# Optimization experiments

Measured on AMD Instinct MI355X. Metric: run time of the kernel, lower is better.

The kernel has to match this reference:

```python
import jax, jax.numpy as jnp
import numpy as np

ALPHA = 0.2   # LeakyReLU negative slope
OF = 64       # out_features


def setup_inputs() -> dict:
    key = jax.random.key(0)
    k1, k2, k3, k4 = jax.random.split(key, 4)
    h = jax.random.normal(k1, (16, 2048, 12, 128), dtype=jnp.float32)
    adj = jax.random.randint(k2, (2, 6, 6), 0, 2, dtype=jnp.int32)
    # learned params (xavier-like scale)
    W = jax.random.normal(k3, (128, 64), dtype=jnp.float32) * 0.1
    a = jax.random.normal(k4, (2, 2 * OF, 1), dtype=jnp.float32) * 0.1
    return {"h": h, "adj": adj, "W": W, "a": a}


def reference(h, adj, W, a):
    # h: [B, N, 12, Fin], adj: [2, 6, 6], W: [Fin, OF], a: [2, 2*OF, 1]
    Wh = jnp.einsum('bnkf,fo->bnko', h, W)  # [B, N, 12, OF]
    outs = []
    for i in range(2):  # fixed 2 chunks of 6 nodes (h.shape[2] // 6)
        chunk = Wh[:, :, i * 6:(i + 1) * 6, :]       # [B, N, 6, OF]
        # matmul(a_input, a[i]) decomposes: e_pq = a1.Wh_p + a2.Wh_q
        a1 = a[i, :OF, 0]
        a2 = a[i, OF:, 0]
        s1 = chunk @ a1                               # [B, N, 6]
        s2 = chunk @ a2                               # [B, N, 6]
        e = jax.nn.leaky_relu(s1[..., :, None] + s2[..., None, :], ALPHA)  # [B,N,6,6]
        ei = e[i]                                     # NOTE: batch index i, as in source
        att = jnp.where(adj[i] > 0, ei, jnp.float32(-9e15))  # [N, 6, 6]
        att = jax.nn.softmax(att, axis=-1)
        # dropout omitted (eval mode)
        outs.append(jnp.einsum('npq,bnqf->bnpf', att, chunk))  # [B, N, 6, OF]
    h_prime = jnp.concatenate(outs, axis=2)           # [B, N, 12, OF]
    return jax.nn.elu(h_prime)                        # concat=True -> ELU
```

## Files before the change

kernel.cpp:

```cpp
#include <hip/hip_runtime.h>
#include <math.h>

#define LRELU_ALPHA 0.2f
#define NEG_BIG -9000000000000000.0f

#define WA_OFF 147456
#define WF_OFF 147968

typedef __attribute__((ext_vector_type(8))) short bf16x8;
typedef __attribute__((ext_vector_type(4))) float f32x4;

static __device__ inline unsigned short f2bf(float x) {
    unsigned int u = __float_as_uint(x);
    unsigned int r = (u + 0x7FFFu + ((u >> 16) & 1u)) >> 16;
    return (unsigned short)r;
}

__global__ __launch_bounds__(256) void gat_prep_kernel(
    const float* __restrict__ W, const float* __restrict__ a,
    float* __restrict__ ws)
{
    const int tid = threadIdx.x;
    if (blockIdx.x < 32) {
        short* wf = (short*)(ws + WF_OFF);
        const int o = blockIdx.x * 256 + tid;
        const int n = o >> 7, k = o & 127;
        wf[o] = (short)f2bf(W[k * 64 + n]);
    } else {
        float* wa = ws + WA_OFF;
        for (int idx = tid; idx < 512; idx += 256) {
            const int gi = idx >> 8, j = (idx >> 7) & 1, c = idx & 127;
            const float* Wr = W + c * 64;
            const float* ar = a + gi * 128 + j * 64;
            float s = 0.f;
#pragma unroll
            for (int f = 0; f < 64; ++f) s = fmaf(Wr[f], ar[f], s);
            wa[idx] = s;
        }
    }
}

__global__ __launch_bounds__(256) void gat_att_kernel(
    const float* __restrict__ h, const int* __restrict__ adj,
    float* __restrict__ ws)
{
    const int warp = threadIdx.x >> 6;
    const int lane = threadIdx.x & 63;
    const int iw = blockIdx.x * 4 + warp;
    const int gi = iw >> 11;
    const int n  = iw & 2047;

    const float* wa = ws + WA_OFF;
    const float2 w1 = *(const float2*)(wa + gi * 256 + 2 * lane);
    const float2 w2 = *(const float2*)(wa + gi * 256 + 128 + 2 * lane);
    const float* hp = h + ((size_t)(gi * 2048 + n) * 12 + (size_t)gi * 6) * 128 + 2 * lane;

    float t1[6], t2[6];
#pragma unroll
    for (int q = 0; q < 6; ++q) {
        const float2 hq = *(const float2*)(hp + q * 128);
        t1[q] = hq.x * w1.x + hq.y * w1.y;
        t2[q] = hq.x * w2.x + hq.y * w2.y;
    }
#pragma unroll
    for (int off = 32; off > 0; off >>= 1) {
#pragma unroll
        for (int q = 0; q < 6; ++q) {
            t1[q] += __shfl_xor(t1[q], off, 64);
            t2[q] += __shfl_xor(t2[q], off, 64);
        }
    }

    if (lane < 6) {
        const int p = lane;
        float s1p = t1[0];
#pragma unroll
        for (int q = 1; q < 6; ++q) { if (p == q) s1p = t1[q]; }

        float row[6];
        float mx = -3.0e38f;
#pragma unroll
        for (int q = 0; q < 6; ++q) {
            float e = s1p + t2[q];
            e = (e > 0.f) ? e : (LRELU_ALPHA * e);
            const int ad = adj[gi * 36 + p * 6 + q];
            const float m = (ad > 0) ? e : NEG_BIG;
            row[q] = m;
            mx = fmaxf(mx, m);
        }
        float sum = 0.f;
#pragma unroll
        for (int q = 0; q < 6; ++q) {
            row[q] = expf(row[q] - mx);
            sum += row[q];
        }
        const float inv = 1.f / sum;
        float* op = ws + (size_t)iw * 36 + p * 6;
#pragma unroll
        for (int q = 0; q < 6; ++q) op[q] = row[q] * inv;
    }
}

#define PSTR 136
__global__ __launch_bounds__(256, 8) void gat_main_mfma(
    const float* __restrict__ h, const float* __restrict__ ws,
    float* __restrict__ out)
{
    __shared__ __align__(16) short Pl[48 * PSTR];
    __shared__ __align__(16) float attl[288];

    const int tid  = threadIdx.x;
    const int warp = tid >> 6;
    const int lane = tid & 63;
    const int half = lane >> 5;
    const int li   = lane & 31;
    const int bn0  = blockIdx.x * 4;
    const int n0   = bn0 & 2047;

    for (int i = tid; i < 288; i += 256) {
        const int gi = i / 144;
        const int rem = i - gi * 144;
        const int nn = rem / 36;
        const int e  = rem - nn * 36;
        attl[i] = ws[(size_t)(gi * 2048 + n0 + nn) * 36 + e];
    }

    const int bn = bn0 + warp;
    const int gi = half;
    const float* hb = h + (size_t)bn * 1536 + gi * 6 * 128 + li * 4;
    f32x4 hv[6];
#pragma unroll
    for (int r = 0; r < 6; ++r)
        hv[r] = __builtin_nontemporal_load((const f32x4*)(hb + r * 128));

    __syncthreads();

    const float* av = attl + gi * 144 + warp * 36;
#pragma unroll
    for (int p = 0; p < 6; ++p) {
        float ax = 0.f, ay = 0.f, az = 0.f, aw = 0.f;
#pragma unroll
        for (int q = 0; q < 6; ++q) {
            const float apq = av[p * 6 + q];
            const f32x4 hq = hv[q];
            ax = fmaf(apq, hq[0], ax);
            ay = fmaf(apq, hq[1], ay);
            az = fmaf(apq, hq[2], az);
            aw = fmaf(apq, hq[3], aw);
        }
        const int row = warp * 12 + gi * 6 + p;
        ushort4 pk;
        pk.x = f2bf(ax); pk.y = f2bf(ay);
        pk.z = f2bf(az); pk.w = f2bf(aw);
        *(ushort4*)(Pl + row * PSTR + li * 4) = pk;
    }

    __syncthreads();

    const short* wf = (const short*)(ws + WF_OFF);
    const int col  = lane & 15;
    const int quad = lane >> 4;
    f32x4 acc[3];
#pragma unroll
    for (int mt = 0; mt < 3; ++mt) acc[mt] = (f32x4){0.f, 0.f, 0.f, 0.f};

#pragma unroll
    for (int ks = 0; ks < 4; ++ks) {
        const bf16x8 bfr = *(const bf16x8*)(wf + (warp * 16 + col) * 128 + ks * 32 + quad * 8);
#pragma unroll
        for (int mt = 0; mt < 3; ++mt) {
            const bf16x8 afr = *(const bf16x8*)(Pl + (mt * 16 + col) * PSTR + ks * 32 + quad * 8);
            acc[mt] = __builtin_amdgcn_mfma_f32_16x16x32_bf16(afr, bfr, acc[mt], 0, 0, 0);
        }
    }

    float* ob = out + (size_t)bn0 * 768 + warp * 16 + col;
#pragma unroll
    for (int mt = 0; mt < 3; ++mt)
#pragma unroll
        for (int r = 0; r < 4; ++r) {
            const int row = mt * 16 + quad * 4 + r;
            float v = acc[mt][r];
            v = (v > 0.f) ? v : (expf(v) - 1.f);
            __builtin_nontemporal_store(v, ob + row * 64);
        }
}

extern "C" void kernel_launch(void* const* d_in, const int* in_sizes, int n_in,
                              void* d_out, int out_size, void* d_ws, size_t ws_size,
                              hipStream_t stream) {
    const float* h   = (const float*)d_in[0];
    const int*   adj = (const int*)d_in[1];
    const float* W   = (const float*)d_in[2];
    const float* a   = (const float*)d_in[3];
    float* out = (float*)d_out;
    float* ws  = (float*)d_ws;

    hipLaunchKernelGGL(gat_prep_kernel, dim3(33), dim3(256), 0, stream, W, a, ws);
    hipLaunchKernelGGL(gat_att_kernel, dim3(1024), dim3(256), 0, stream, h, adj, ws);
    hipLaunchKernelGGL(gat_main_mfma, dim3(8192), dim3(256), 0, stream, h, ws, out);
}
```

Before: 316.2 us.

## Fuse attention softmax computation into main MFMA kernel, dropping separate launch

Removes the standalone attention kernel and has each block of the main kernel compute the 6x6 softmax attention rows it needs directly into shared memory. The workspace layout for the precomputed W·a vectors and the bf16 W is compacted to the start of the buffer. This cuts one kernel launch and the global round trip of the attention matrix, and drops one block barrier. In exchange, attention for batches 0 and 1 is recomputed redundantly by every batch's blocks, re-reading the corresponding h rows, which should mostly be served from cache.

```diff
diff --git a/kernel.cpp b/kernel.cpp
--- a/kernel.cpp
+++ b/kernel.cpp
@@ -4,8 +4,8 @@
 #define LRELU_ALPHA 0.2f
 #define NEG_BIG -9000000000000000.0f
 
-#define WA_OFF 147456
-#define WF_OFF 147968
+#define WA_OFF 0
+#define WF_OFF 512
 
 typedef __attribute__((ext_vector_type(8))) short bf16x8;
 typedef __attribute__((ext_vector_type(4))) float f32x4;
@@ -40,71 +40,10 @@
     }
 }
 
-__global__ __launch_bounds__(256) void gat_att_kernel(
-    const float* __restrict__ h, const int* __restrict__ adj,
-    float* __restrict__ ws)
-{
-    const int warp = threadIdx.x >> 6;
-    const int lane = threadIdx.x & 63;
-    const int iw = blockIdx.x * 4 + warp;
-    const int gi = iw >> 11;
-    const int n  = iw & 2047;
-
-    const float* wa = ws + WA_OFF;
-    const float2 w1 = *(const float2*)(wa + gi * 256 + 2 * lane);
-    const float2 w2 = *(const float2*)(wa + gi * 256 + 128 + 2 * lane);
-    const float* hp = h + ((size_t)(gi * 2048 + n) * 12 + (size_t)gi * 6) * 128 + 2 * lane;
-
-    float t1[6], t2[6];
-#pragma unroll
-    for (int q = 0; q < 6; ++q) {
-        const float2 hq = *(const float2*)(hp + q * 128);
-        t1[q] = hq.x * w1.x + hq.y * w1.y;
-        t2[q] = hq.x * w2.x + hq.y * w2.y;
-    }
-#pragma unroll
-    for (int off = 32; off > 0; off >>= 1) {
-#pragma unroll
-        for (int q = 0; q < 6; ++q) {
-            t1[q] += __shfl_xor(t1[q], off, 64);
-            t2[q] += __shfl_xor(t2[q], off, 64);
-        }
-    }
-
-    if (lane < 6) {
-        const int p = lane;
-        float s1p = t1[0];
-#pragma unroll
-        for (int q = 1; q < 6; ++q) { if (p == q) s1p = t1[q]; }
-
-        float row[6];
-        float mx = -3.0e38f;
-#pragma unroll
-        for (int q = 0; q < 6; ++q) {
-            float e = s1p + t2[q];
-            e = (e > 0.f) ? e : (LRELU_ALPHA * e);
-            const int ad = adj[gi * 36 + p * 6 + q];
-            const float m = (ad > 0) ? e : NEG_BIG;
-            row[q] = m;
-            mx = fmaxf(mx, m);
-        }
-        float sum = 0.f;
-#pragma unroll
-        for (int q = 0; q < 6; ++q) {
-            row[q] = expf(row[q] - mx);
-            sum += row[q];
-        }
-        const float inv = 1.f / sum;
-        float* op = ws + (size_t)iw * 36 + p * 6;
-#pragma unroll
-        for (int q = 0; q < 6; ++q) op[q] = row[q] * inv;
-    }
-}
-
 #define PSTR 136
 __global__ __launch_bounds__(256, 8) void gat_main_mfma(
-    const float* __restrict__ h, const float* __restrict__ ws,
-    float* __restrict__ out)
+    const float* __restrict__ h, const int* __restrict__ adj,
+    const float* __restrict__ ws, float* __restrict__ out)
 {
     __shared__ __align__(16) short Pl[48 * PSTR];
     __shared__ __align__(16) float attl[288];
@@ -116,24 +55,64 @@
     const int li   = lane & 31;
     const int bn0  = blockIdx.x * 4;
     const int n0   = bn0 & 2047;
+    const int gi   = half;
 
-    for (int i = tid; i < 288; i += 256) {
-        const int gi = i / 144;
-        const int rem = i - gi * 144;
-        const int nn = rem / 36;
-        const int e  = rem - nn * 36;
-        attl[i] = ws[(size_t)(gi * 2048 + n0 + nn) * 36 + e];
+    {
+        const int n = n0 + warp;
+        const float* wa = ws + WA_OFF;
+        const f32x4 w1 = *(const f32x4*)(wa + gi * 256 + li * 4);
+        const f32x4 w2 = *(const f32x4*)(wa + gi * 256 + 128 + li * 4);
+        const float* hs = h + (size_t)(gi * 2048 + n) * 1536 + gi * 6 * 128 + li * 4;
+        float t1[6], t2[6];
+#pragma unroll
+        for (int q = 0; q < 6; ++q) {
+            const f32x4 hq = *(const f32x4*)(hs + q * 128);
+            t1[q] = hq[0] * w1[0] + hq[1] * w1[1] + hq[2] * w1[2] + hq[3] * w1[3];
+            t2[q] = hq[0] * w2[0] + hq[1] * w2[1] + hq[2] * w2[2] + hq[3] * w2[3];
+        }
+#pragma unroll
+        for (int off = 16; off > 0; off >>= 1) {
+#pragma unroll
+            for (int q = 0; q < 6; ++q) {
+                t1[q] += __shfl_xor(t1[q], off, 64);
+                t2[q] += __shfl_xor(t2[q], off, 64);
+            }
+        }
+        if (li < 6) {
+            const int p = li;
+            float s1p = t1[0];
+#pragma unroll
+            for (int q = 1; q < 6; ++q) { if (p == q) s1p = t1[q]; }
+            float row[6];
+            float mx = -3.0e38f;
+#pragma unroll
+            for (int q = 0; q < 6; ++q) {
+                float e = s1p + t2[q];
+                e = (e > 0.f) ? e : (LRELU_ALPHA * e);
+                const int ad = adj[gi * 36 + p * 6 + q];
+                const float m = (ad > 0) ? e : NEG_BIG;
+                row[q] = m;
+                mx = fmaxf(mx, m);
+            }
+            float sum = 0.f;
+#pragma unroll
+            for (int q = 0; q < 6; ++q) {
+                row[q] = expf(row[q] - mx);
+                sum += row[q];
+            }
+            const float inv = 1.f / sum;
+#pragma unroll
+            for (int q = 0; q < 6; ++q)
+                attl[gi * 144 + warp * 36 + p * 6 + q] = row[q] * inv;
+        }
     }
 
     const int bn = bn0 + warp;
-    const int gi = half;
     const float* hb = h + (size_t)bn * 1536 + gi * 6 * 128 + li * 4;
     f32x4 hv[6];
 #pragma unroll
     for (int r = 0; r < 6; ++r)
         hv[r] = __builtin_nontemporal_load((const f32x4*)(hb + r * 128));
-
-    __syncthreads();
 
     const float* av = attl + gi * 144 + warp * 36;
 #pragma unroll
@@ -197,6 +176,5 @@
     float* ws  = (float*)d_ws;
 
     hipLaunchKernelGGL(gat_prep_kernel, dim3(33), dim3(256), 0, stream, W, a, ws);
-    hipLaunchKernelGGL(gat_att_kernel, dim3(1024), dim3(256), 0, stream, h, adj, ws);
-    hipLaunchKernelGGL(gat_main_mfma, dim3(8192), dim3(256), 0, stream, h, ws, out);
+    hipLaunchKernelGGL(gat_main_mfma, dim3(8192), dim3(256), 0, stream, h, adj, ws, out);
 }
```

After: 317.8 us. Within noise of the previous version (+0.5%).
